# Optimization experiments

Measured on AMD Instinct MI355X. Metric: run time of the kernel, lower is better.

Reference implementation:

```python
import jax, jax.numpy as jnp
import numpy as np

N_NODES = 100000
N_RELS = 500
N_EDGES = 1000000
IN_DIM = 64
OUT_DIM = 64
BN_EPS = 1e-5


def _bn(v, gamma, beta):
    # BatchNorm1d in training mode: batch mean / biased variance
    m = jnp.mean(v, axis=0)
    var = jnp.var(v, axis=0)
    return (v - m) * jax.lax.rsqrt(var + BN_EPS) * gamma + beta


def setup_inputs() -> dict:
    key = jax.random.key(0)
    ks = jax.random.split(key, 12)
    inp = {
        "x": jax.random.normal(ks[0], (N_NODES, IN_DIM), dtype=jnp.float32),
        "r": jax.random.normal(ks[1], (N_RELS, IN_DIM), dtype=jnp.float32),
        "que_context": jax.random.normal(ks[2], (OUT_DIM,), dtype=jnp.float32),
        "edge_index": jax.random.randint(ks[3], (2, N_EDGES), 0, N_NODES),
        "edge_attr": jax.random.randint(ks[4], (N_EDGES,), 0, N_RELS),
        "edge_type": jax.random.randint(ks[5], (N_EDGES,), 0, N_RELS),
        # mess_trans: Linear(2*in_dim -> out_dim)
        "W_m": jax.random.normal(ks[6], (OUT_DIM, 2 * IN_DIM), dtype=jnp.float32) * 0.05,
        "b_m": jnp.zeros((OUT_DIM,), dtype=jnp.float32),
        # atten_weight: [2*out_dim] (stored as [1, 2*out_dim] in torch)
        "atten_w": jax.random.normal(ks[7], (2 * OUT_DIM,), dtype=jnp.float32) * 0.1,
        # rel_trans: Linear(in_dim -> out_dim)
        "W_r": jax.random.normal(ks[8], (OUT_DIM, IN_DIM), dtype=jnp.float32) * 0.05,
        "b_r": jnp.zeros((OUT_DIM,), dtype=jnp.float32),
        # batchnorm affine params
        "e_gamma": jnp.ones((OUT_DIM,), dtype=jnp.float32),
        "e_beta": jnp.zeros((OUT_DIM,), dtype=jnp.float32),
        "r_gamma": jnp.ones((OUT_DIM,), dtype=jnp.float32),
        "r_beta": jnp.zeros((OUT_DIM,), dtype=jnp.float32),
    }
    return inp


def reference(x, r, que_context, edge_index, edge_attr, edge_type,
              W_m, b_m, atten_w, W_r, b_r, e_gamma, e_beta, r_gamma, r_beta):
    src = edge_index[0]  # [E]
    tgt = edge_index[1]  # [E]

    # gather source-node and edge-relation embeddings, linear message transform
    source_embeds = x[src]            # [E, in_dim]
    edge_rel_embeds = r[edge_attr]    # [E, in_dim]
    messages = jnp.concatenate([source_embeds, edge_rel_embeds], axis=1) @ W_m.T + b_m  # [E, out_dim]

    # edge-wise attention score: <atten_w, [messages ; que_context]>
    # split dot product to avoid materializing the concat
    aw_m, aw_q = atten_w[:OUT_DIM], atten_w[OUT_DIM:]
    atten = messages @ aw_m + jnp.dot(aw_q, que_context)  # [E]
    atten = jnp.exp(jnp.tanh(atten))

    # scatter-sum normalization (softmax-like over incoming edges)
    coeffs_sum = jax.ops.segment_sum(atten, tgt, num_segments=N_NODES)  # [N]
    weights = atten / coeffs_sum[tgt]                                   # [E]

    # weighted scatter-sum aggregation
    x_new = jax.ops.segment_sum(messages * weights[:, None], tgt, num_segments=N_NODES)  # [N, out_dim]
    x_new = jnp.tanh(_bn(x_new, e_gamma, e_beta))  # dropout = identity (eval)

    r_new = jnp.tanh(_bn(r @ W_r.T + b_r, r_gamma, r_beta))
    return (x_new, r_new)
```

## Files before the change

kernel.cpp:

```cpp
#include <hip/hip_runtime.h>
#include <hip/hip_fp16.h>

#define N_NODES 100000
#define N_RELS  500
#define N_EDGES 1000000
#define SRCMASK 131071

#define OFF_C     0
#define OFF_SUMS  64
#define OFF_SUMSQ 128
#define OFF_RSUM  320
#define OFF_RSQ   384
#define OFF_SR    576
#define OFF_RP    1088
#define OFF_SX    33152
#define OFF_DEG   133152
#define OFF_OFF   233216
#define OFF_META  333248
#define OFF_PRH   2333248
#define OFF_PXH   2349280
#define OFF_ACCH  5549280
#define OFF_PART  8749280

typedef _Float16 h8 __attribute__((ext_vector_type(8)));
typedef float f4 __attribute__((ext_vector_type(4)));

__global__ void __launch_bounds__(256) k_rel(const float* __restrict__ r, const float* __restrict__ Wm,
                                             const float* __restrict__ Wr, const float* __restrict__ br,
                                             const float* __restrict__ aw, const float* __restrict__ bm,
                                             const float* __restrict__ que, float* __restrict__ ws) {
    __shared__ float wm[64][65];
    __shared__ float wr[64][65];
    __shared__ float awl[64];
    int tid = threadIdx.x;
    for (int i = tid; i < 4096; i += 256) {
        int row = i >> 6, col = i & 63;
        wm[row][col] = Wm[row * 128 + 64 + col];
        wr[row][col] = Wr[row * 64 + col];
    }
    if (tid < 64) awl[tid] = aw[tid];
    __syncthreads();
    int lane = tid & 63, wv = tid >> 6;
    int i = blockIdx.x * 4 + wv;
    float rv = r[i * 64 + lane];
    float p = 0.f, q = br[lane];
#pragma unroll
    for (int k = 0; k < 64; ++k) {
        float rk = __shfl(rv, k);
        p += wm[lane][k] * rk;
        q += wr[lane][k] * rk;
    }
    __half* prh = (__half*)(ws + OFF_PRH);
    prh[i * 64 + lane] = __float2half(p);
    ws[OFF_RP + i * 64 + lane] = q;
    atomicAdd(&ws[OFF_RSUM + lane], q);
    atomicAdd(&ws[OFF_RSQ + lane], q * q);
    float t = p * awl[lane];
    for (int o = 32; o > 0; o >>= 1) t += __shfl_down(t, o);
    if (lane == 0) ws[OFF_SR + i] = t;
    if (blockIdx.x == 0 && tid < 64) {
        float v = aw[tid] * bm[tid] + aw[64 + tid] * que[tid];
        for (int o = 32; o > 0; o >>= 1) v += __shfl_down(v, o);
        if (tid == 0) ws[OFF_C] = v;
    }
}

__global__ void __launch_bounds__(128) k_px(const float* __restrict__ x, const float* __restrict__ Wm,
                                            const float* __restrict__ aw, float* __restrict__ ws) {
    int tid = threadIdx.x;
    int lane = tid & 63, wv = tid >> 6;
    int wtile = blockIdx.x * 2 + wv;
    int n0 = wtile * 16;
    int rrow = lane & 15, grp = lane >> 4;

    h8 bfr[4][2];
    float awv[4];
#pragma unroll
    for (int ct = 0; ct < 4; ++ct) {
        int col = ct * 16 + rrow;
        awv[ct] = aw[col];
        const float* wp = Wm + col * 128;
#pragma unroll
        for (int h = 0; h < 2; ++h) {
            f4 w0 = *(const f4*)(wp + h * 32 + grp * 8);
            f4 w1 = *(const f4*)(wp + h * 32 + grp * 8 + 4);
            h8 b;
#pragma unroll
            for (int j = 0; j < 4; ++j) { b[j] = (_Float16)w0[j]; b[4 + j] = (_Float16)w1[j]; }
            bfr[ct][h] = b;
        }
    }
    const float* xp = x + (size_t)(n0 + rrow) * 64;
    h8 afr[2];
#pragma unroll
    for (int h = 0; h < 2; ++h) {
        f4 a0 = *(const f4*)(xp + h * 32 + grp * 8);
        f4 a1 = *(const f4*)(xp + h * 32 + grp * 8 + 4);
        h8 a;
#pragma unroll
        for (int j = 0; j < 4; ++j) { a[j] = (_Float16)a0[j]; a[4 + j] = (_Float16)a1[j]; }
        afr[h] = a;
    }
    f4 acc[4];
#pragma unroll
    for (int ct = 0; ct < 4; ++ct) acc[ct] = (f4){0.f, 0.f, 0.f, 0.f};
#pragma unroll
    for (int h = 0; h < 2; ++h)
#pragma unroll
        for (int ct = 0; ct < 4; ++ct)
            acc[ct] = __builtin_amdgcn_mfma_f32_16x16x32_f16(afr[h], bfr[ct][h], acc[ct], 0, 0, 0);

    __half* pxh = (__half*)(ws + OFF_PXH);
#pragma unroll
    for (int q = 0; q < 4; ++q) {
        int node = n0 + grp * 4 + q;
#pragma unroll
        for (int ct = 0; ct < 4; ++ct)
            pxh[(size_t)node * 64 + ct * 16 + rrow] = __float2half(acc[ct][q]);
        float t = acc[0][q] * awv[0] + acc[1][q] * awv[1] + acc[2][q] * awv[2] + acc[3][q] * awv[3];
        t += __shfl_xor(t, 1); t += __shfl_xor(t, 2); t += __shfl_xor(t, 4); t += __shfl_xor(t, 8);
        if (rrow == 0) ws[OFF_SX + node] = t;
    }
}

__global__ void __launch_bounds__(256) k_hist(const int* __restrict__ ei, int* __restrict__ deg) {
    int e = blockIdx.x * 256 + threadIdx.x;
    if (e >= N_EDGES) return;
    atomicAdd(&deg[ei[N_EDGES + e]], 1);
}

__global__ void __launch_bounds__(256) k_scan1(const int* __restrict__ deg, int* __restrict__ off,
                                               int* __restrict__ part) {
    __shared__ int ts[256];
    int tid = threadIdx.x;
    int idx0 = blockIdx.x * 1000 + tid * 4;
    int4 d = make_int4(0, 0, 0, 0);
    if (tid < 250) d = *(const int4*)(deg + idx0);
    int s = d.x + d.y + d.z + d.w;
    ts[tid] = s;
    __syncthreads();
    for (int o = 1; o < 256; o <<= 1) {
        int v = (tid >= o) ? ts[tid - o] : 0;
        __syncthreads();
        ts[tid] += v;
        __syncthreads();
    }
    int excl = ts[tid] - s;
    if (tid < 250) {
        off[idx0] = excl;
        off[idx0 + 1] = excl + d.x;
        off[idx0 + 2] = excl + d.x + d.y;
        off[idx0 + 3] = excl + d.x + d.y + d.z;
    }
    if (tid == 255) part[blockIdx.x] = ts[255];
}

__global__ void __launch_bounds__(128) k_scan2(int* __restrict__ part, int* __restrict__ off) {
    __shared__ int ts[128];
    int tid = threadIdx.x;
    int v = (tid < 100) ? part[tid] : 0;
    ts[tid] = v;
    __syncthreads();
    for (int o = 1; o < 128; o <<= 1) {
        int u = (tid >= o) ? ts[tid - o] : 0;
        __syncthreads();
        ts[tid] += u;
        __syncthreads();
    }
    if (tid < 100) part[tid] = ts[tid] - v;
    if (tid == 127) off[N_NODES] = ts[127];
}

__global__ void __launch_bounds__(256) k_scan3(int* __restrict__ off, const int* __restrict__ part,
                                               int* __restrict__ cursor) {
    int i = blockIdx.x * 256 + threadIdx.x;
    if (i >= N_NODES) return;
    int v = off[i] + part[i / 1000];
    off[i] = v;
    cursor[i] = v;
}

__global__ void __launch_bounds__(256) k_scatter(const int* __restrict__ ei, const int* __restrict__ ea,
                                                 const float* __restrict__ ws, int* __restrict__ cursor,
                                                 uint2* __restrict__ meta) {
    int e = blockIdx.x * 256 + threadIdx.x;
    if (e >= N_EDGES) return;
    int src = ei[e], tgt = ei[N_EDGES + e], at = ea[e];
    float a = __expf(tanhf(ws[OFF_SX + src] + ws[OFF_SR + at] + ws[OFF_C]));
    int pos = atomicAdd(&cursor[tgt], 1);
    meta[pos] = make_uint2(__float_as_uint(a), (unsigned)src | ((unsigned)at << 17));
}

__global__ void __launch_bounds__(256) k_main(const int* __restrict__ off, const uint2* __restrict__ meta,
                                              const float* __restrict__ bm, float* __restrict__ ws) {
    __shared__ float bsum[64], bsq[64];
    int tid = threadIdx.x;
    int lane = tid & 63, wv = tid >> 6;
    if (tid < 64) { bsum[tid] = 0.f; bsq[tid] = 0.f; }
    __syncthreads();
    const __half* pxh = (const __half*)(ws + OFF_PXH);
    const __half* prh = (const __half*)(ws + OFF_PRH);
    __half* acch = (__half*)(ws + OFF_ACCH);
    float bm_l = bm[lane];
    float ls = 0.f, lq = 0.f;
    int t0 = blockIdx.x * 32 + wv * 8;
#pragma unroll 1
    for (int g = 0; g < 8; ++g) {
        int t = t0 + g;
        int s = off[t], e = off[t + 1];
        float acc = 0.f, asum = 0.f;
        int i = s;
        for (; i + 4 <= e; i += 4) {
            uint2 m0 = meta[i], m1 = meta[i + 1], m2 = meta[i + 2], m3 = meta[i + 3];
            float px0 = __half2float(pxh[(size_t)(m0.y & SRCMASK) * 64 + lane]);
            float pr0 = __half2float(prh[(m0.y >> 17) * 64 + lane]);
            float px1 = __half2float(pxh[(size_t)(m1.y & SRCMASK) * 64 + lane]);
            float pr1 = __half2float(prh[(m1.y >> 17) * 64 + lane]);
            float px2 = __half2float(pxh[(size_t)(m2.y & SRCMASK) * 64 + lane]);
            float pr2 = __half2float(prh[(m2.y >> 17) * 64 + lane]);
            float px3 = __half2float(pxh[(size_t)(m3.y & SRCMASK) * 64 + lane]);
            float pr3 = __half2float(prh[(m3.y >> 17) * 64 + lane]);
            float a0 = __uint_as_float(m0.x), a1 = __uint_as_float(m1.x);
            float a2 = __uint_as_float(m2.x), a3 = __uint_as_float(m3.x);
            acc += a0 * (px0 + pr0) + a1 * (px1 + pr1) + a2 * (px2 + pr2) + a3 * (px3 + pr3);
            asum += (a0 + a1) + (a2 + a3);
        }
        for (; i < e; ++i) {
            uint2 mv = meta[i];
            float a = __uint_as_float(mv.x);
            float pxv = __half2float(pxh[(size_t)(mv.y & SRCMASK) * 64 + lane]);
            float prv = __half2float(prh[(mv.y >> 17) * 64 + lane]);
            acc += a * (pxv + prv);
            asum += a;
        }
        float p = (e > s) ? (acc / asum + bm_l) : 0.f;
        acch[(size_t)t * 64 + lane] = __float2half(p);
        ls += p;
        lq += p * p;
    }
    atomicAdd(&bsum[lane], ls);
    atomicAdd(&bsq[lane], lq);
    __syncthreads();
    if (tid < 64) {
        atomicAdd(&ws[OFF_SUMS + tid], bsum[tid]);
        atomicAdd(&ws[OFF_SUMSQ + tid], bsq[tid]);
    }
}

__global__ void __launch_bounds__(256) k_xout(const float* __restrict__ ws, const float* __restrict__ eg,
                                              const float* __restrict__ eb, float* __restrict__ out) {
    __shared__ float sc[64], sh[64];
    int tid = threadIdx.x;
    if (tid < 64) {
        float mean = ws[OFF_SUMS + tid] * (1.f / N_NODES);
        float var = ws[OFF_SUMSQ + tid] * (1.f / N_NODES) - mean * mean;
        float s = rsqrtf(var + 1e-5f) * eg[tid];
        sc[tid] = s;
        sh[tid] = eb[tid] - mean * s;
    }
    __syncthreads();
    int lane = tid & 63, wv = tid >> 6;
    const __half* acch = (const __half*)(ws + OFF_ACCH);
    int base = blockIdx.x * 64;
    for (int it = 0; it < 16; ++it) {
        int t = base + it * 4 + wv;
        if (t < N_NODES) {
            float p = __half2float(acch[(size_t)t * 64 + lane]);
            out[(size_t)t * 64 + lane] = tanhf(p * sc[lane] + sh[lane]);
        }
    }
}

__global__ void __launch_bounds__(256) k_rout(const float* __restrict__ ws, const float* __restrict__ rg,
                                              const float* __restrict__ rb, float* __restrict__ out) {
    __shared__ float sc[64], sh[64];
    int tid = threadIdx.x;
    if (tid < 64) {
        float mean = ws[OFF_RSUM + tid] * (1.f / N_RELS);
        float var = ws[OFF_RSQ + tid] * (1.f / N_RELS) - mean * mean;
        float s = rsqrtf(var + 1e-5f) * rg[tid];
        sc[tid] = s;
        sh[tid] = rb[tid] - mean * s;
    }
    __syncthreads();
    int lane = tid & 63, wv = tid >> 6;
    int i = blockIdx.x * 4 + wv;
    float p = ws[OFF_RP + i * 64 + lane];
    out[(size_t)N_NODES * 64 + (size_t)i * 64 + lane] = tanhf(p * sc[lane] + sh[lane]);
}

extern "C" void kernel_launch(void* const* d_in, const int* in_sizes, int n_in,
                              void* d_out, int out_size, void* d_ws, size_t ws_size,
                              hipStream_t stream) {
    const float* x   = (const float*)d_in[0];
    const float* r   = (const float*)d_in[1];
    const float* que = (const float*)d_in[2];
    const int*   ei  = (const int*)d_in[3];
    const int*   ea  = (const int*)d_in[4];
    const float* Wm  = (const float*)d_in[6];
    const float* bm  = (const float*)d_in[7];
    const float* aw  = (const float*)d_in[8];
    const float* Wr  = (const float*)d_in[9];
    const float* br  = (const float*)d_in[10];
    const float* eg  = (const float*)d_in[11];
    const float* eb  = (const float*)d_in[12];
    const float* rg  = (const float*)d_in[13];
    const float* rb  = (const float*)d_in[14];
    float* out = (float*)d_out;
    float* ws  = (float*)d_ws;
    int*   deg  = (int*)(ws + OFF_DEG);
    int*   off  = (int*)(ws + OFF_OFF);
    int*   part = (int*)(ws + OFF_PART);
    uint2* meta = (uint2*)(ws + OFF_META);

    hipMemsetAsync(ws + OFF_SUMS, 0, 512 * sizeof(float), stream);
    hipMemsetAsync(deg, 0, (size_t)N_NODES * sizeof(int), stream);

    k_rel<<<125, 256, 0, stream>>>(r, Wm, Wr, br, aw, bm, que, ws);
    k_px<<<3125, 128, 0, stream>>>(x, Wm, aw, ws);
    k_hist<<<(N_EDGES + 255) / 256, 256, 0, stream>>>(ei, deg);
    k_scan1<<<100, 256, 0, stream>>>(deg, off, part);
    k_scan2<<<1, 128, 0, stream>>>(part, off);
    k_scan3<<<(N_NODES + 255) / 256, 256, 0, stream>>>(off, part, deg);
    k_scatter<<<(N_EDGES + 255) / 256, 256, 0, stream>>>(ei, ea, ws, deg, meta);
    k_main<<<3125, 256, 0, stream>>>(off, meta, bm, ws);
    k_xout<<<(N_NODES + 63) / 64, 256, 0, stream>>>(ws, eg, eb, out);
    k_rout<<<125, 256, 0, stream>>>(ws, rg, rb, out);
}
```

Measured before the change: 364.5 us.

## Split each wavefront into two half-waves gathering half2 rows, fuse rel output into xout

The gather loop in k_main now has each half of a wavefront process a different edge, with each lane loading a __half2 (two features) per row. Two edges' rows are fetched per wave instruction, and the halves are combined with a cross-lane shuffle. This aims to double memory-level parallelism per gather instruction and halve loop iterations for the irregular pxh/prh row loads. Separately, the relation BatchNorm/tanh output kernel is folded into k_xout to save one launch. The cost is extra shuffles and a masked tail loop that may waste half a wave on odd degrees.

```diff
diff --git a/kernel.cpp b/kernel.cpp
--- a/kernel.cpp
+++ b/kernel.cpp
@@ -201,45 +201,68 @@
     const __half* pxh = (const __half*)(ws + OFF_PXH);
     const __half* prh = (const __half*)(ws + OFF_PRH);
     __half* acch = (__half*)(ws + OFF_ACCH);
-    float bm_l = bm[lane];
-    float ls = 0.f, lq = 0.f;
+    int ld = lane & 31, hf = lane >> 5;
+    float2 bm2 = *(const float2*)(bm + 2 * ld);
+    float ls0 = 0.f, ls1 = 0.f, lq0 = 0.f, lq1 = 0.f;
     int t0 = blockIdx.x * 32 + wv * 8;
 #pragma unroll 1
     for (int g = 0; g < 8; ++g) {
         int t = t0 + g;
         int s = off[t], e = off[t + 1];
-        float acc = 0.f, asum = 0.f;
+        float ax = 0.f, ay = 0.f, asum = 0.f;
         int i = s;
-        for (; i + 4 <= e; i += 4) {
-            uint2 m0 = meta[i], m1 = meta[i + 1], m2 = meta[i + 2], m3 = meta[i + 3];
-            float px0 = __half2float(pxh[(size_t)(m0.y & SRCMASK) * 64 + lane]);
-            float pr0 = __half2float(prh[(m0.y >> 17) * 64 + lane]);
-            float px1 = __half2float(pxh[(size_t)(m1.y & SRCMASK) * 64 + lane]);
-            float pr1 = __half2float(prh[(m1.y >> 17) * 64 + lane]);
-            float px2 = __half2float(pxh[(size_t)(m2.y & SRCMASK) * 64 + lane]);
-            float pr2 = __half2float(prh[(m2.y >> 17) * 64 + lane]);
-            float px3 = __half2float(pxh[(size_t)(m3.y & SRCMASK) * 64 + lane]);
-            float pr3 = __half2float(prh[(m3.y >> 17) * 64 + lane]);
+        for (; i + 8 <= e; i += 8) {
+            uint2 m0 = meta[i + 0 + hf], m1 = meta[i + 2 + hf];
+            uint2 m2 = meta[i + 4 + hf], m3 = meta[i + 6 + hf];
+            float2 p0 = __half22float2(*(const __half2*)(pxh + (size_t)(m0.y & SRCMASK) * 64 + 2 * ld));
+            float2 q0 = __half22float2(*(const __half2*)(prh + (m0.y >> 17) * 64 + 2 * ld));
+            float2 p1 = __half22float2(*(const __half2*)(pxh + (size_t)(m1.y & SRCMASK) * 64 + 2 * ld));
+            float2 q1 = __half22float2(*(const __half2*)(prh + (m1.y >> 17) * 64 + 2 * ld));
+            float2 p2 = __half22float2(*(const __half2*)(pxh + (size_t)(m2.y & SRCMASK) * 64 + 2 * ld));
+            float2 q2 = __half22float2(*(const __half2*)(prh + (m2.y >> 17) * 64 + 2 * ld));
+            float2 p3 = __half22float2(*(const __half2*)(pxh + (size_t)(m3.y & SRCMASK) * 64 + 2 * ld));
+            float2 q3 = __half22float2(*(const __half2*)(prh + (m3.y >> 17) * 64 + 2 * ld));
             float a0 = __uint_as_float(m0.x), a1 = __uint_as_float(m1.x);
             float a2 = __uint_as_float(m2.x), a3 = __uint_as_float(m3.x);
-            acc += a0 * (px0 + pr0) + a1 * (px1 + pr1) + a2 * (px2 + pr2) + a3 * (px3 + pr3);
+            ax += a0 * (p0.x + q0.x) + a1 * (p1.x + q1.x) + a2 * (p2.x + q2.x) + a3 * (p3.x + q3.x);
+            ay += a0 * (p0.y + q0.y) + a1 * (p1.y + q1.y) + a2 * (p2.y + q2.y) + a3 * (p3.y + q3.y);
             asum += (a0 + a1) + (a2 + a3);
         }
-        for (; i < e; ++i) {
-            uint2 mv = meta[i];
-            float a = __uint_as_float(mv.x);
-            float pxv = __half2float(pxh[(size_t)(mv.y & SRCMASK) * 64 + lane]);
-            float prv = __half2float(prh[(mv.y >> 17) * 64 + lane]);
-            acc += a * (pxv + prv);
+        for (; i < e; i += 2) {
+            int j = i + hf;
+            bool valid = j < e;
+            uint2 m = meta[valid ? j : (e - 1)];
+            float a = valid ? __uint_as_float(m.x) : 0.f;
+            float2 p = __half22float2(*(const __half2*)(pxh + (size_t)(m.y & SRCMASK) * 64 + 2 * ld));
+            float2 q = __half22float2(*(const __half2*)(prh + (m.y >> 17) * 64 + 2 * ld));
+            ax += a * (p.x + q.x);
+            ay += a * (p.y + q.y);
             asum += a;
         }
-        float p = (e > s) ? (acc / asum + bm_l) : 0.f;
-        acch[(size_t)t * 64 + lane] = __float2half(p);
-        ls += p;
-        lq += p * p;
-    }
-    atomicAdd(&bsum[lane], ls);
-    atomicAdd(&bsq[lane], lq);
+        ax += __shfl_xor(ax, 32);
+        ay += __shfl_xor(ay, 32);
+        asum += __shfl_xor(asum, 32);
+        float vx, vy;
+        if (e > s) {
+            float inv = 1.f / asum;
+            vx = ax * inv + bm2.x;
+            vy = ay * inv + bm2.y;
+        } else { vx = 0.f; vy = 0.f; }
+        if (hf == 0) {
+            __half2 h2;
+            h2.x = __float2half(vx);
+            h2.y = __float2half(vy);
+            *(__half2*)(acch + (size_t)t * 64 + 2 * ld) = h2;
+        }
+        ls0 += vx; lq0 += vx * vx;
+        ls1 += vy; lq1 += vy * vy;
+    }
+    if (hf == 0) {
+        atomicAdd(&bsum[2 * ld], ls0);
+        atomicAdd(&bsq[2 * ld], lq0);
+        atomicAdd(&bsum[2 * ld + 1], ls1);
+        atomicAdd(&bsq[2 * ld + 1], lq1);
+    }
     __syncthreads();
     if (tid < 64) {
         atomicAdd(&ws[OFF_SUMS + tid], bsum[tid]);
@@ -248,8 +271,9 @@
 }
 
 __global__ void __launch_bounds__(256) k_xout(const float* __restrict__ ws, const float* __restrict__ eg,
-                                              const float* __restrict__ eb, float* __restrict__ out) {
-    __shared__ float sc[64], sh[64];
+                                              const float* __restrict__ eb, const float* __restrict__ rg,
+                                              const float* __restrict__ rb, float* __restrict__ out) {
+    __shared__ float sc[64], sh[64], rsc[64], rsh[64];
     int tid = threadIdx.x;
     if (tid < 64) {
         float mean = ws[OFF_SUMS + tid] * (1.f / N_NODES);
@@ -257,6 +281,11 @@
         float s = rsqrtf(var + 1e-5f) * eg[tid];
         sc[tid] = s;
         sh[tid] = eb[tid] - mean * s;
+        float rmean = ws[OFF_RSUM + tid] * (1.f / N_RELS);
+        float rvar = ws[OFF_RSQ + tid] * (1.f / N_RELS) - rmean * rmean;
+        float rs = rsqrtf(rvar + 1e-5f) * rg[tid];
+        rsc[tid] = rs;
+        rsh[tid] = rb[tid] - rmean * rs;
     }
     __syncthreads();
     int lane = tid & 63, wv = tid >> 6;
@@ -269,24 +298,11 @@
             out[(size_t)t * 64 + lane] = tanhf(p * sc[lane] + sh[lane]);
         }
     }
-}
-
-__global__ void __launch_bounds__(256) k_rout(const float* __restrict__ ws, const float* __restrict__ rg,
-                                              const float* __restrict__ rb, float* __restrict__ out) {
-    __shared__ float sc[64], sh[64];
-    int tid = threadIdx.x;
-    if (tid < 64) {
-        float mean = ws[OFF_RSUM + tid] * (1.f / N_RELS);
-        float var = ws[OFF_RSQ + tid] * (1.f / N_RELS) - mean * mean;
-        float s = rsqrtf(var + 1e-5f) * rg[tid];
-        sc[tid] = s;
-        sh[tid] = rb[tid] - mean * s;
-    }
-    __syncthreads();
-    int lane = tid & 63, wv = tid >> 6;
-    int i = blockIdx.x * 4 + wv;
-    float p = ws[OFF_RP + i * 64 + lane];
-    out[(size_t)N_NODES * 64 + (size_t)i * 64 + lane] = tanhf(p * sc[lane] + sh[lane]);
+    if (blockIdx.x < 125) {
+        int i = blockIdx.x * 4 + wv;
+        float p = ws[OFF_RP + i * 64 + lane];
+        out[(size_t)N_NODES * 64 + (size_t)i * 64 + lane] = tanhf(p * rsc[lane] + rsh[lane]);
+    }
 }
 
 extern "C" void kernel_launch(void* const* d_in, const int* in_sizes, int n_in,
@@ -324,6 +340,5 @@
     k_scan3<<<(N_NODES + 255) / 256, 256, 0, stream>>>(off, part, deg);
     k_scatter<<<(N_EDGES + 255) / 256, 256, 0, stream>>>(ei, ea, ws, deg, meta);
     k_main<<<3125, 256, 0, stream>>>(off, meta, bm, ws);
-    k_xout<<<(N_NODES + 63) / 64, 256, 0, stream>>>(ws, eg, eb, out);
-    k_rout<<<125, 256, 0, stream>>>(ws, rg, rb, out);
-}
+    k_xout<<<(N_NODES + 63) / 64, 256, 0, stream>>>(ws, eg, eb, rg, rb, out);
+}
```

New measurement: 367.8 us. No clear change (+0.9%).
